# Kernel optimization log

Hardware: AMD Instinct MI355X
Metric: run time of the kernel (lower is better)

## Reference

```python
import jax, jax.numpy as jnp
import numpy as np

NUM_HEADS = 16
NEG_INF = float('-inf')


def setup_inputs() -> dict:
    key = jax.random.key(0)
    ks = jax.random.split(key, 8)
    B, S, D = 2, 2048, 1024
    return {
        "query": jax.random.normal(ks[0], (B, S, D), jnp.float32),
        "key": jax.random.normal(ks[1], (B, S, D), jnp.float32),
        "value": jax.random.normal(ks[2], (B, S, D), jnp.float32),
        "attention_mask": jnp.zeros((B, S, S), dtype=bool),
        "Wq": jax.random.normal(ks[3], (D, D), jnp.float32) * (D ** -0.5),
        "Wk": jax.random.normal(ks[4], (D, D), jnp.float32) * (D ** -0.5),
        "Wv": jax.random.normal(ks[5], (D, D), jnp.float32) * (D ** -0.5),
        "Wout": jax.random.normal(ks[6], (D, D), jnp.float32) * (D ** -0.5),
        "b_out": jnp.zeros((D,), jnp.float32),
        "is_causal": 1,
    }


def reference(query, key, value, attention_mask, Wq, Wk, Wv, Wout, b_out, is_causal):
    B, q_len, D = query.shape
    k_len = key.shape[1]
    H = NUM_HEADS
    dk = D // H
    # projections (torch Linear: x @ W.T), split heads -> [B, H, S, dk]
    q = (query @ Wq.T).reshape(B, q_len, H, dk).transpose(0, 2, 1, 3)
    k = (key @ Wk.T).reshape(B, k_len, H, dk).transpose(0, 2, 1, 3)
    v = (value @ Wv.T).reshape(B, k_len, H, dk).transpose(0, 2, 1, 3)
    scores = jnp.einsum('bhqd,bhkd->bhqk', q, k) / jnp.sqrt(jnp.float32(dk))
    if is_causal:
        causal = jnp.triu(jnp.ones((q_len, k_len), dtype=bool), k=1)
        scores = jnp.where(causal, NEG_INF, scores)
    # attn_mask True -> masked out; broadcast over heads
    scores = jnp.where(attention_mask[:, None, :, :], NEG_INF, scores)
    attn = jax.nn.softmax(scores, axis=-1)
    attn = jnp.where(jnp.isnan(attn), 0.0, attn)  # fully-masked rows -> 0
    out = jnp.einsum('bhqk,bhkd->bhqd', attn, v)
    out = out.transpose(0, 2, 1, 3).reshape(B, q_len, D)
    return out @ Wout.T + b_out
```

## Files before the change

kernel.cpp:

```cpp
#include <hip/hip_runtime.h>
#include <hip/hip_bf16.h>

typedef __attribute__((ext_vector_type(8))) short bf16x8;
typedef __attribute__((ext_vector_type(4))) float f32x4;
typedef unsigned long long u64;
typedef unsigned int u32;

#define MFMA(a,b,c) __builtin_amdgcn_mfma_f32_16x16x32_bf16(a,b,c,0,0,0)
#define NEG_INF (-__builtin_inff())
#define SCALE2 0.1803368801111244f

__device__ __forceinline__ unsigned short f2b(float f) {
  unsigned int u = __float_as_uint(f);
  u = u + 0x7fffu + ((u >> 16) & 1u);
  return (unsigned short)(u >> 16);
}

__device__ __forceinline__ u32 pkbf(float lo, float hi) {
  __hip_bfloat162 h = __float22bfloat162_rn(float2{lo, hi});
  return *reinterpret_cast<u32*>(&h);
}

__device__ __forceinline__ void gload_lds16(const unsigned short* g, unsigned short* l) {
  __builtin_amdgcn_global_load_lds((const __attribute__((address_space(1))) void*)g,
                                   (__attribute__((address_space(3))) void*)l, 16, 0, 0);
}

__global__ void cvt7(const float* s0, const float* s1, const float* s2,
                     const float* s3, const float* s4, const float* s5, const float* s6,
                     unsigned short* d0, unsigned short* d1, unsigned short* d2,
                     unsigned short* d3, unsigned short* d4, unsigned short* d5, unsigned short* d6,
                     int nbig, int nsmall) {
  const float* s; unsigned short* d; int n4;
  switch (blockIdx.y) {
    case 0: s=s0; d=d0; n4=nbig; break;
    case 1: s=s1; d=d1; n4=nbig; break;
    case 2: s=s2; d=d2; n4=nbig; break;
    case 3: s=s3; d=d3; n4=nsmall; break;
    case 4: s=s4; d=d4; n4=nsmall; break;
    case 5: s=s5; d=d5; n4=nsmall; break;
    default: s=s6; d=d6; n4=nsmall; break;
  }
  int i = blockIdx.x * blockDim.x + threadIdx.x;
  if (i < n4) {
    float4 v = reinterpret_cast<const float4*>(s)[i];
    ushort4 o;
    o.x = f2b(v.x); o.y = f2b(v.y); o.z = f2b(v.z); o.w = f2b(v.w);
    reinterpret_cast<ushort4*>(d)[i] = o;
  }
}

__global__ void pack_mask(const unsigned char* __restrict__ am, u64* __restrict__ pm, int nU) {
  int lane = threadIdx.x & 63;
  int wid = blockIdx.x * (blockDim.x >> 6) + (threadIdx.x >> 6);
  int stride = gridDim.x * (blockDim.x >> 6);
  for (int u = wid; u < nU; u += stride) {
    unsigned char v = am[(size_t)u * 64 + lane];
    u64 m = __ballot(v != 0);
    if (lane == 0) pm[u] = m;
  }
}

__global__ void mask_summary(const u64* __restrict__ pm, u32* __restrict__ ms, int rows, int nkt) {
  int lane = threadIdx.x & 63;
  int wid = (blockIdx.x * blockDim.x + threadIdx.x) >> 6;
  int nw = (gridDim.x * blockDim.x) >> 6;
  for (int rp = wid; rp < (rows >> 1); rp += nw) {
    int row = rp * 2 + (lane >> 5);
    int t = lane & 31;
    u64 v = pm[(size_t)row * nkt + t];
    u64 bm = __ballot(v != 0ULL);
    if (lane == 0)  ms[rp*2]     = (u32)bm;
    if (lane == 32) ms[rp*2 + 1] = (u32)(bm >> 32);
  }
}

__global__ __launch_bounds__(256) void qkv64(
    const unsigned short* __restrict__ A,
    const unsigned short* __restrict__ Bw,
    unsigned short* __restrict__ Cqk,
    unsigned short* __restrict__ Cv)
{
  const int K = 1024;
  __shared__ unsigned short As[64*32];
  __shared__ unsigned short Bs[128*32];
  const int tid  = threadIdx.x;
  const int w    = tid >> 6, lane = tid & 63;
  const int wr   = w >> 1,   wc   = w & 1;
  const int g    = lane >> 4, li  = lane & 15;
  const int m0   = blockIdx.x * 64, n0 = blockIdx.y * 128;
  const int bq0  = (m0 >> 12) * 1024 + n0;

  f32x4 acc[2][4] = {};
  const int crow = lane >> 2, ccol = (lane & 3) * 8;
  const unsigned short* gA  = A  + (size_t)(m0 + w*16 + crow)*K + ccol;
  const unsigned short* gB0 = Bw + (size_t)(bq0 + w*16 + crow)*K + ccol;
  const unsigned short* gB1 = Bw + (size_t)(bq0 + (w+4)*16 + crow)*K + ccol;

  for (int k0 = 0; k0 < K; k0 += 32) {
    gload_lds16(gA  + k0, &As[w*512]);
    gload_lds16(gB0 + k0, &Bs[w*512]);
    gload_lds16(gB1 + k0, &Bs[(w+4)*512]);
    __syncthreads();

    bf16x8 af[2], bf[4];
    #pragma unroll
    for (int i = 0; i < 2; ++i)
      af[i] = *(const bf16x8*)(&As[(wr*32 + i*16 + li)*32 + g*8]);
    #pragma unroll
    for (int j = 0; j < 4; ++j)
      bf[j] = *(const bf16x8*)(&Bs[(wc*64 + j*16 + li)*32 + g*8]);
    #pragma unroll
    for (int i = 0; i < 2; ++i)
      #pragma unroll
      for (int j = 0; j < 4; ++j)
        acc[i][j] = MFMA(af[i], bf[j], acc[i][j]);
    __syncthreads();
  }

  #pragma unroll
  for (int i = 0; i < 2; ++i) {
    #pragma unroll
    for (int j = 0; j < 4; ++j) {
      int col = n0 + wc*64 + j*16 + li;
      #pragma unroll
      for (int r = 0; r < 4; ++r) {
        int row = m0 + wr*32 + i*16 + g*4 + r;
        float v = acc[i][j][r];
        if (row < 8192) {
          size_t addr = (((size_t)(row >> 11) * 16 + (col >> 6)) * 2048 + (row & 2047)) * 64 + (col & 63);
          Cqk[addr] = f2b(v);
        } else {
          int t = row & 4095;
          size_t addr = (((size_t)(t >> 11) * 16 + (col >> 6)) * 64 + (col & 63)) * 2048 + (t & 2047);
          Cv[addr] = f2b(v);
        }
      }
    }
  }
}

__global__ __launch_bounds__(256) void gemm64f(
    const unsigned short* __restrict__ A,
    const unsigned short* __restrict__ Bw,
    float* __restrict__ Cf,
    const float* __restrict__ bias,
    int M, int N, int K)
{
  __shared__ unsigned short As[64*32];
  __shared__ unsigned short Bs[128*32];
  const int tid  = threadIdx.x;
  const int w    = tid >> 6, lane = tid & 63;
  const int wr   = w >> 1,   wc   = w & 1;
  const int g    = lane >> 4, li  = lane & 15;
  const int m0   = blockIdx.x * 64, n0 = blockIdx.y * 128;

  f32x4 acc[2][4] = {};
  const int crow = lane >> 2, ccol = (lane & 3) * 8;
  const unsigned short* gA  = A  + (size_t)(m0 + w*16 + crow)*K + ccol;
  const unsigned short* gB0 = Bw + (size_t)(n0 + w*16 + crow)*K + ccol;
  const unsigned short* gB1 = Bw + (size_t)(n0 + (w+4)*16 + crow)*K + ccol;

  for (int k0 = 0; k0 < K; k0 += 32) {
    gload_lds16(gA  + k0, &As[w*512]);
    gload_lds16(gB0 + k0, &Bs[w*512]);
    gload_lds16(gB1 + k0, &Bs[(w+4)*512]);
    __syncthreads();

    bf16x8 af[2], bf[4];
    #pragma unroll
    for (int i = 0; i < 2; ++i)
      af[i] = *(const bf16x8*)(&As[(wr*32 + i*16 + li)*32 + g*8]);
    #pragma unroll
    for (int j = 0; j < 4; ++j)
      bf[j] = *(const bf16x8*)(&Bs[(wc*64 + j*16 + li)*32 + g*8]);
    #pragma unroll
    for (int i = 0; i < 2; ++i)
      #pragma unroll
      for (int j = 0; j < 4; ++j)
        acc[i][j] = MFMA(af[i], bf[j], acc[i][j]);
    __syncthreads();
  }

  #pragma unroll
  for (int i = 0; i < 2; ++i) {
    #pragma unroll
    for (int j = 0; j < 4; ++j) {
      int col = n0 + wc*64 + j*16 + li;
      #pragma unroll
      for (int r = 0; r < 4; ++r) {
        int row = m0 + wr*32 + i*16 + g*4 + r;
        Cf[(size_t)row*N + col] = acc[i][j][r] + bias[col];
      }
    }
  }
}

__global__ __launch_bounds__(256, 4) void attn_kernel(
    const unsigned short* __restrict__ Qh,
    const unsigned short* __restrict__ Kh,
    const unsigned short* __restrict__ Vt,
    const u64* __restrict__ pmask,
    const u32* __restrict__ msum,
    const int* __restrict__ causal_p,
    unsigned short* __restrict__ Ob,
    int B, int H, int S)
{
  __shared__ unsigned short Ks [64*64];
  __shared__ unsigned short Vts[64*64];

  const int tid = threadIdx.x, w = tid >> 6, lane = tid & 63;
  const int g = lane >> 4, li = lane & 15;
  const int nkt = S >> 6, nqt = S >> 6;
  const int causal = causal_p[0];

  int id = blockIdx.x;
  int par = (id ^ (id >> 8)) & 1;
  int qh  = ((id >> 1) & 15) ^ (((id >> 8) & 3) << 2);
  int bh  = id >> 5;
  int qt  = par ? (nqt - 1 - qh) : qh;
  const int q0 = qt << 6;
  const int b = bh / H, h = bh % H;
  const size_t baseK = (size_t)bh * S * 64;
  const size_t baseV = (size_t)bh * 64 * S;

  const int qg = q0 + w*16 + li;
  const unsigned short* qp = Qh + baseK + (size_t)qg*64 + g*8;
  const bf16x8 qf0 = *(const bf16x8*)(qp);
  const bf16x8 qf1 = *(const bf16x8*)(qp + 32);

  const u32 sOr = msum[(size_t)b*S + qg];

  f32x4 oacc[4] = {};
  float mrun = -1e30f, lrun = 0.f;

  const int colk  = (lane & 7) ^ ((lane >> 3) & 7);
  const int ldrow = lane >> 3;
  const int ntile = causal ? (qt + 1) : nkt;

  for (int t = 0; t < ntile; ++t) {
    const int kv0 = t << 6;
    __syncthreads();
    #pragma unroll
    for (int s2 = 0; s2 < 2; ++s2) {
      int u = w*2 + s2;
      gload_lds16(Kh + baseK + (size_t)(kv0 + u*8 + ldrow)*64 + colk*8, &Ks[u*512]);
      gload_lds16(Vt + baseV + (size_t)(u*8 + ldrow)*S + kv0 + colk*8, &Vts[u*512]);
    }
    __syncthreads();

    f32x4 sa[4];
    #pragma unroll
    for (int ni = 0; ni < 4; ++ni) sa[ni] = (f32x4){0.f, 0.f, 0.f, 0.f};
    #pragma unroll
    for (int ni = 0; ni < 4; ++ni) {
      int row = ni*16 + li, rx = row & 7;
      bf16x8 k0 = *(const bf16x8*)(&Ks[row*64 + ((g     ^ rx))*8]);
      bf16x8 k1 = *(const bf16x8*)(&Ks[row*64 + (((4+g) ^ rx))*8]);
      sa[ni] = MFMA(k0, qf0, sa[ni]);
      sa[ni] = MFMA(k1, qf1, sa[ni]);
    }

    const bool edge   = (causal != 0) && (t == ntile - 1);
    const bool doMask = __any(((sOr >> t) & 1u) != 0u);
    float corr;

    if (!edge && !doMask) {
      float mx = sa[0][0];
      #pragma unroll
      for (int ni = 0; ni < 4; ++ni)
        #pragma unroll
        for (int r = 0; r < 4; ++r)
          if (ni + r) mx = fmaxf(mx, sa[ni][r]);
      mx = fmaxf(mx, __shfl_xor(mx, 16));
      mx = fmaxf(mx, __shfl_xor(mx, 32));
      float mu = fmaxf(mrun, mx * SCALE2);
      corr = exp2f(mrun - mu);
      float rs = 0.f;
      #pragma unroll
      for (int ni = 0; ni < 4; ++ni)
        #pragma unroll
        for (int r = 0; r < 4; ++r) {
          float pe = exp2f(fmaf(sa[ni][r], SCALE2, -mu));
          sa[ni][r] = pe;
          rs += pe;
        }
      rs += __shfl_xor(rs, 16);
      rs += __shfl_xor(rs, 32);
      lrun = lrun * corr + rs;
      mrun = mu;
    } else {
      u64 mrow = doMask ? pmask[((size_t)b*S + qg) * nkt + t] : 0ULL;
      #pragma unroll
      for (int ni = 0; ni < 4; ++ni)
        #pragma unroll
        for (int r = 0; r < 4; ++r) {
          int kvloc = ni*16 + g*4 + r;
          bool dead = (edge && (kv0 + kvloc > qg)) || ((mrow >> kvloc) & 1ULL);
          sa[ni][r] = dead ? NEG_INF : sa[ni][r] * SCALE2;
        }
      float mx = sa[0][0];
      #pragma unroll
      for (int ni = 0; ni < 4; ++ni)
        #pragma unroll
        for (int r = 0; r < 4; ++r)
          if (ni + r) mx = fmaxf(mx, sa[ni][r]);
      mx = fmaxf(mx, __shfl_xor(mx, 16));
      mx = fmaxf(mx, __shfl_xor(mx, 32));
      float mu = fmaxf(mrun, mx);
      corr = exp2f(mrun - mu);
      float rs = 0.f;
      #pragma unroll
      for (int ni = 0; ni < 4; ++ni)
        #pragma unroll
        for (int r = 0; r < 4; ++r) {
          float pe = exp2f(sa[ni][r] - mu);
          sa[ni][r] = pe;
          rs += pe;
        }
      rs += __shfl_xor(rs, 16);
      rs += __shfl_xor(rs, 32);
      lrun = lrun * corr + rs;
      mrun = mu;
    }

    bf16x8 pf[2];
    #pragma unroll
    for (int c = 0; c < 2; ++c) {
      u32 PA0 = pkbf(sa[2*c  ][0], sa[2*c  ][1]);
      u32 PA1 = pkbf(sa[2*c  ][2], sa[2*c  ][3]);
      u32 PB0 = pkbf(sa[2*c+1][0], sa[2*c+1][1]);
      u32 PB1 = pkbf(sa[2*c+1][2], sa[2*c+1][3]);
      u32 X16_0 = (u32)__shfl_xor((int)((g==2) ? PB0 : PA0), 16);
      u32 X16_1 = (u32)__shfl_xor((int)((g==2) ? PB1 : PA1), 16);
      u32 X32_0 = (u32)__shfl_xor((int)((g==0) ? PB0 : PA0), 32);
      u32 X32_1 = (u32)__shfl_xor((int)((g==0) ? PB1 : PA1), 32);
      u32 X48_0 = (u32)__shfl_xor((int)((g==1) ? PB0 : PA0), 48);
      u32 X48_1 = (u32)__shfl_xor((int)((g==1) ? PB1 : PA1), 48);
      union { u32 u[4]; bf16x8 v; } pbu;
      pbu.u[0] = (g==0) ? PA0   : (g==1) ? X48_0 : (g==2) ? X32_0 : X16_0;
      pbu.u[1] = (g==0) ? PA1   : (g==1) ? X48_1 : (g==2) ? X32_1 : X16_1;
      pbu.u[2] = (g==0) ? X16_0 : (g==1) ? X32_0 : (g==2) ? X48_0 : PB0;
      pbu.u[3] = (g==0) ? X16_1 : (g==1) ? X32_1 : (g==2) ? X48_1 : PB1;
      pf[c] = pbu.v;
    }

    #pragma unroll
    for (int di = 0; di < 4; ++di) {
      oacc[di][0] *= corr; oacc[di][1] *= corr;
      oacc[di][2] *= corr; oacc[di][3] *= corr;
    }

    #pragma unroll
    for (int c = 0; c < 2; ++c) {
      #pragma unroll
      for (int di = 0; di < 4; ++di) {
        int d = di*16 + li;
        bf16x8 vf = *(const bf16x8*)(&Vts[d*64 + (((c*4+g) ^ (d&7)))*8]);
        oacc[di] = MFMA(vf, pf[c], oacc[di]);
      }
    }
  }

  __syncthreads();
  unsigned short* scr = &Ks[w*1024];
  float rl = (lrun > 0.f) ? 1.0f / lrun : 0.f;
  #pragma unroll
  for (int di = 0; di < 4; ++di)
    #pragma unroll
    for (int r = 0; r < 4; ++r) {
      int d = di*16 + g*4 + r;
      scr[li*64 + (((d>>3) ^ (li&7)))*8 + (d&7)] = f2b(oacc[di][r] * rl);
    }
  const int D = H * 64;
  #pragma unroll
  for (int rr = 0; rr < 2; ++rr) {
    int q = rr*8 + (lane >> 3);
    int sl = lane & 7;
    bf16x8 v = *(const bf16x8*)(&scr[q*64 + ((sl ^ (q & 7)))*8]);
    *(bf16x8*)(Ob + (size_t)(b*S + q0 + w*16 + q)*D + h*64 + sl*8) = v;
  }
}

extern "C" void kernel_launch(void* const* d_in, const int* in_sizes, int n_in,
                              void* d_out, int out_size, void* d_ws, size_t ws_size,
                              hipStream_t stream) {
  const float* query = (const float*)d_in[0];
  const float* key_  = (const float*)d_in[1];
  const float* value = (const float*)d_in[2];
  const unsigned char* amask = (const unsigned char*)d_in[3];
  const float* Wq   = (const float*)d_in[4];
  const float* Wk   = (const float*)d_in[5];
  const float* Wv   = (const float*)d_in[6];
  const float* Wout = (const float*)d_in[7];
  const float* b_out = (const float*)d_in[8];
  const int* is_causal = (const int*)d_in[9];
  float* out = (float*)d_out;

  const int B = 2, S = 2048, D = 1024, H = 16;
  const int M = B * S;
  const size_t nx = (size_t)M * D;
  const size_t nw = (size_t)D * D;
  const int nU = B * S * (S / 64);

  unsigned short* ws = (unsigned short*)d_ws;
  unsigned short* xq = ws;
  unsigned short* xk = xq + nx;
  unsigned short* xv = xk + nx;
  unsigned short* wq = xv + nx;
  unsigned short* wk = wq + nw;
  unsigned short* wv = wk + nw;
  unsigned short* wo = wv + nw;
  unsigned short* qb = wo + nw;
  unsigned short* kb = qb + nx;
  unsigned short* vt = kb + nx;
  u32* msum = (u32*)(vt + nx);
  unsigned short* ob = xq;
  u64* pmask = (u64*)xv;

  cvt7<<<dim3((unsigned)(nx/4/256), 7), 256, 0, stream>>>(
      query, key_, value, Wq, Wk, Wv, Wout,
      xq, xk, xv, wq, wk, wv, wo, (int)(nx/4), (int)(nw/4));

  qkv64<<<dim3(3*M/64, D/128), 256, 0, stream>>>(xq, wq, qb, vt);

  pack_mask<<<512, 256, 0, stream>>>(amask, pmask, nU);
  mask_summary<<<128, 256, 0, stream>>>(pmask, msum, M, S/64);

  attn_kernel<<<dim3((S/64) * B * H), 256, 0, stream>>>(qb, kb, vt, pmask, msum, is_causal, ob, B, H, S);

  gemm64f<<<dim3(M/64, D/128), 256, 0, stream>>>(ob, wo, out, b_out, M, D, D);
}
```

Measured before the change: 186.5 us.

## Double-buffer LDS in projection GEMMs and enlarge QKV tile to 128x128

Both the QKV projection GEMM and the output projection GEMM now keep two LDS buffers. The next K-slice is loaded asynchronously into one buffer while MFMAs run on the other, and the load before compute is replaced by a prologue plus a prefetch inside the loop. The QKV kernel also grows its M tile from 64 to 128, so each wave holds a 4x4 accumulator block, which raises data reuse per LDS load and halves the grid. The costs are more registers and LDS per block, which may reduce occupancy, and fewer blocks for the QKV launch.

Measured after the change: 172.9 us. -7.3%, faster.

```diff
diff --git a/kernel.cpp b/kernel.cpp
--- a/kernel.cpp
+++ b/kernel.cpp
@@ -75,43 +75,56 @@
   }
 }
 
-__global__ __launch_bounds__(256) void qkv64(
+__global__ __launch_bounds__(256) void qkv128(
     const unsigned short* __restrict__ A,
     const unsigned short* __restrict__ Bw,
     unsigned short* __restrict__ Cqk,
     unsigned short* __restrict__ Cv)
 {
-  const int K = 1024;
-  __shared__ unsigned short As[64*32];
-  __shared__ unsigned short Bs[128*32];
+  const int K = 1024, NT = 32;
+  __shared__ unsigned short As[2][128*32];
+  __shared__ unsigned short Bs[2][128*32];
   const int tid  = threadIdx.x;
   const int w    = tid >> 6, lane = tid & 63;
   const int wr   = w >> 1,   wc   = w & 1;
   const int g    = lane >> 4, li  = lane & 15;
-  const int m0   = blockIdx.x * 64, n0 = blockIdx.y * 128;
+  const int m0   = blockIdx.x * 128, n0 = blockIdx.y * 128;
   const int bq0  = (m0 >> 12) * 1024 + n0;
 
-  f32x4 acc[2][4] = {};
-  const int crow = lane >> 2, ccol = (lane & 3) * 8;
-  const unsigned short* gA  = A  + (size_t)(m0 + w*16 + crow)*K + ccol;
-  const unsigned short* gB0 = Bw + (size_t)(bq0 + w*16 + crow)*K + ccol;
-  const unsigned short* gB1 = Bw + (size_t)(bq0 + (w+4)*16 + crow)*K + ccol;
-
-  for (int k0 = 0; k0 < K; k0 += 32) {
-    gload_lds16(gA  + k0, &As[w*512]);
-    gload_lds16(gB0 + k0, &Bs[w*512]);
-    gload_lds16(gB1 + k0, &Bs[(w+4)*512]);
-    __syncthreads();
-
-    bf16x8 af[2], bf[4];
-    #pragma unroll
-    for (int i = 0; i < 2; ++i)
-      af[i] = *(const bf16x8*)(&As[(wr*32 + i*16 + li)*32 + g*8]);
+  f32x4 acc[4][4] = {};
+
+  const int rS0 = (w*2+0)*16 + (lane>>2);
+  const int rS1 = (w*2+1)*16 + (lane>>2);
+  const int cS  = (lane&3)*8;
+  const unsigned short* gA0 = A  + (size_t)(m0+rS0)*K + cS;
+  const unsigned short* gA1 = A  + (size_t)(m0+rS1)*K + cS;
+  const unsigned short* gB0 = Bw + (size_t)(bq0+rS0)*K + cS;
+  const unsigned short* gB1 = Bw + (size_t)(bq0+rS1)*K + cS;
+
+  gload_lds16(gA0, &As[0][(w*2+0)*512]);
+  gload_lds16(gA1, &As[0][(w*2+1)*512]);
+  gload_lds16(gB0, &Bs[0][(w*2+0)*512]);
+  gload_lds16(gB1, &Bs[0][(w*2+1)*512]);
+  __syncthreads();
+
+  for (int t = 0; t < NT; ++t) {
+    const int cur = t & 1;
+    if (t + 1 < NT) {
+      const int k1 = (t + 1) * 32;
+      gload_lds16(gA0 + k1, &As[cur^1][(w*2+0)*512]);
+      gload_lds16(gA1 + k1, &As[cur^1][(w*2+1)*512]);
+      gload_lds16(gB0 + k1, &Bs[cur^1][(w*2+0)*512]);
+      gload_lds16(gB1 + k1, &Bs[cur^1][(w*2+1)*512]);
+    }
+    bf16x8 af[4], bf[4];
+    #pragma unroll
+    for (int i = 0; i < 4; ++i)
+      af[i] = *(const bf16x8*)(&As[cur][(wr*64 + i*16 + li)*32 + g*8]);
     #pragma unroll
     for (int j = 0; j < 4; ++j)
-      bf[j] = *(const bf16x8*)(&Bs[(wc*64 + j*16 + li)*32 + g*8]);
-    #pragma unroll
-    for (int i = 0; i < 2; ++i)
+      bf[j] = *(const bf16x8*)(&Bs[cur][(wc*64 + j*16 + li)*32 + g*8]);
+    #pragma unroll
+    for (int i = 0; i < 4; ++i)
       #pragma unroll
       for (int j = 0; j < 4; ++j)
         acc[i][j] = MFMA(af[i], bf[j], acc[i][j]);
@@ -119,20 +132,20 @@
   }
 
   #pragma unroll
-  for (int i = 0; i < 2; ++i) {
+  for (int i = 0; i < 4; ++i) {
     #pragma unroll
     for (int j = 0; j < 4; ++j) {
       int col = n0 + wc*64 + j*16 + li;
       #pragma unroll
       for (int r = 0; r < 4; ++r) {
-        int row = m0 + wr*32 + i*16 + g*4 + r;
+        int row = m0 + wr*64 + i*16 + g*4 + r;
         float v = acc[i][j][r];
         if (row < 8192) {
           size_t addr = (((size_t)(row >> 11) * 16 + (col >> 6)) * 2048 + (row & 2047)) * 64 + (col & 63);
           Cqk[addr] = f2b(v);
         } else {
-          int t = row & 4095;
-          size_t addr = (((size_t)(t >> 11) * 16 + (col >> 6)) * 64 + (col & 63)) * 2048 + (t & 2047);
+          int tk = row & 4095;
+          size_t addr = (((size_t)(tk >> 11) * 16 + (col >> 6)) * 64 + (col & 63)) * 2048 + (tk & 2047);
           Cv[addr] = f2b(v);
         }
       }
@@ -140,15 +153,16 @@
   }
 }
 
-__global__ __launch_bounds__(256) void gemm64f(
+__global__ __launch_bounds__(256) void gemm64db(
     const unsigned short* __restrict__ A,
     const unsigned short* __restrict__ Bw,
     float* __restrict__ Cf,
     const float* __restrict__ bias,
     int M, int N, int K)
 {
-  __shared__ unsigned short As[64*32];
-  __shared__ unsigned short Bs[128*32];
+  const int NT = 32;
+  __shared__ unsigned short As[2][64*32];
+  __shared__ unsigned short Bs[2][128*32];
   const int tid  = threadIdx.x;
   const int w    = tid >> 6, lane = tid & 63;
   const int wr   = w >> 1,   wc   = w & 1;
@@ -161,19 +175,26 @@
   const unsigned short* gB0 = Bw + (size_t)(n0 + w*16 + crow)*K + ccol;
   const unsigned short* gB1 = Bw + (size_t)(n0 + (w+4)*16 + crow)*K + ccol;
 
-  for (int k0 = 0; k0 < K; k0 += 32) {
-    gload_lds16(gA  + k0, &As[w*512]);
-    gload_lds16(gB0 + k0, &Bs[w*512]);
-    gload_lds16(gB1 + k0, &Bs[(w+4)*512]);
-    __syncthreads();
-
+  gload_lds16(gA,  &As[0][w*512]);
+  gload_lds16(gB0, &Bs[0][w*512]);
+  gload_lds16(gB1, &Bs[0][(w+4)*512]);
+  __syncthreads();
+
+  for (int t = 0; t < NT; ++t) {
+    const int cur = t & 1;
+    if (t + 1 < NT) {
+      const int k1 = (t + 1) * 32;
+      gload_lds16(gA  + k1, &As[cur^1][w*512]);
+      gload_lds16(gB0 + k1, &Bs[cur^1][w*512]);
+      gload_lds16(gB1 + k1, &Bs[cur^1][(w+4)*512]);
+    }
     bf16x8 af[2], bf[4];
     #pragma unroll
     for (int i = 0; i < 2; ++i)
-      af[i] = *(const bf16x8*)(&As[(wr*32 + i*16 + li)*32 + g*8]);
+      af[i] = *(const bf16x8*)(&As[cur][(wr*32 + i*16 + li)*32 + g*8]);
     #pragma unroll
     for (int j = 0; j < 4; ++j)
-      bf[j] = *(const bf16x8*)(&Bs[(wc*64 + j*16 + li)*32 + g*8]);
+      bf[j] = *(const bf16x8*)(&Bs[cur][(wc*64 + j*16 + li)*32 + g*8]);
     #pragma unroll
     for (int i = 0; i < 2; ++i)
       #pragma unroll
@@ -422,12 +443,12 @@
       query, key_, value, Wq, Wk, Wv, Wout,
       xq, xk, xv, wq, wk, wv, wo, (int)(nx/4), (int)(nw/4));
 
-  qkv64<<<dim3(3*M/64, D/128), 256, 0, stream>>>(xq, wq, qb, vt);
+  qkv128<<<dim3(3*M/128, D/128), 256, 0, stream>>>(xq, wq, qb, vt);
 
   pack_mask<<<512, 256, 0, stream>>>(amask, pmask, nU);
   mask_summary<<<128, 256, 0, stream>>>(pmask, msum, M, S/64);
 
   attn_kernel<<<dim3((S/64) * B * H), 256, 0, stream>>>(qb, kb, vt, pmask, msum, is_causal, ob, B, H, S);
 
-  gemm64f<<<dim3(M/64, D/128), 256, 0, stream>>>(ob, wo, out, b_out, M, D, D);
-}
+  gemm64db<<<dim3(M/64, D/128), 256, 0, stream>>>(ob, wo, out, b_out, M, D, D);
+}
```
